# Kernel optimization log

Hardware: AMD Instinct MI355X
Metric: run time of the kernel (lower is better)

Reference implementation:

```python
import jax, jax.numpy as jnp
from jax import lax
import numpy as np

IMG_H, IMG_W = 800.0, 1344.0
NMS_PRE, NMS_POST, MAX_NUM = 2000, 1000, 1000
IOU_THR = 0.7
STRIDES = [4, 8, 16, 32, 64]
SIZES = [(200, 336), (100, 168), (50, 84), (25, 42), (13, 21)]
MAX_RATIO = float(abs(np.log(16.0 / 1000.0)))  # mmdet wh_ratio_clip


def _make_anchors(H, W, stride):
    # mmdet AnchorGenerator: scales=[8], ratios=[0.5,1,2], base_size=stride
    ratios = np.array([0.5, 1.0, 2.0])
    scale = 8.0
    hr = np.sqrt(ratios)
    wr = 1.0 / hr
    ws = stride * wr * scale
    hs = stride * hr * scale
    c = stride / 2.0
    base = np.stack([c - 0.5 * ws, c - 0.5 * hs, c + 0.5 * ws, c + 0.5 * hs], 1)  # [3,4]
    xx, yy = np.meshgrid(np.arange(W) * stride, np.arange(H) * stride)
    shifts = np.stack([xx, yy, xx, yy], -1).reshape(-1, 1, 4)  # [H*W,1,4]
    return (shifts + base[None]).reshape(-1, 4).astype(np.float32)  # order (H,W,A)


def setup_inputs() -> dict:
    key = jax.random.key(0)
    inp = {}
    for i, (H, W) in enumerate(SIZES):
        k1, k2, key = jax.random.split(key, 3)
        inp[f"cls{i}"] = jax.random.normal(k1, (2, 3, H, W), jnp.float32)
        inp[f"bbox{i}"] = jax.random.normal(k2, (2, 12, H, W), jnp.float32) * 0.5
        inp[f"anc{i}"] = jnp.asarray(_make_anchors(H, W, STRIDES[i]))
    return inp


def _delta2bbox(deltas, anchors):
    # deltas, anchors: [..., 4]; means=0, stds=1
    dx, dy = deltas[..., 0], deltas[..., 1]
    dw = jnp.clip(deltas[..., 2], -MAX_RATIO, MAX_RATIO)
    dh = jnp.clip(deltas[..., 3], -MAX_RATIO, MAX_RATIO)
    pw = anchors[..., 2] - anchors[..., 0]
    ph = anchors[..., 3] - anchors[..., 1]
    px = (anchors[..., 0] + anchors[..., 2]) * 0.5
    py = (anchors[..., 1] + anchors[..., 3]) * 0.5
    gw = pw * jnp.exp(dw)
    gh = ph * jnp.exp(dh)
    gx = px + pw * dx
    gy = py + ph * dy
    x1 = jnp.clip(gx - 0.5 * gw, 0.0, IMG_W)
    y1 = jnp.clip(gy - 0.5 * gh, 0.0, IMG_H)
    x2 = jnp.clip(gx + 0.5 * gw, 0.0, IMG_W)
    y2 = jnp.clip(gy + 0.5 * gh, 0.0, IMG_H)
    return jnp.stack([x1, y1, x2, y2], axis=-1)


def _pairwise_iou(b):
    # b: [N,4]
    area = (b[:, 2] - b[:, 0]) * (b[:, 3] - b[:, 1])
    lt = jnp.maximum(b[:, None, :2], b[None, :, :2])
    rb = jnp.minimum(b[:, None, 2:], b[None, :, 2:])
    wh = jnp.clip(rb - lt, 0.0, None)
    inter = wh[..., 0] * wh[..., 1]
    union = area[:, None] + area[None, :] - inter
    return inter / jnp.maximum(union, 1e-6)


def _nms_single(boxes, scores):
    # boxes [NMS_PRE,4], scores [NMS_PRE] (one image). Greedy NMS, keep NMS_POST.
    N = scores.shape[0]
    order = jnp.argsort(-scores)
    b = boxes[order]
    s = scores[order]
    iou = _pairwise_iou(lax.stop_gradient(b))
    idx = jnp.arange(N)

    def step(supp, i):
        keep_i = jnp.logical_not(supp[i])
        supp = supp | (keep_i & (iou[i] > IOU_THR) & (idx > i))
        return supp, keep_i

    _, keeps = lax.scan(step, jnp.zeros((N,), bool), idx)
    s_kept = jnp.where(keeps, s, -1.0)
    top_s, top_i = lax.top_k(s_kept, NMS_POST)
    return b[top_i], top_s


def _process_level(cls, bbox, anchors):
    B = cls.shape[0]
    # [B,A,H,W] -> [B,H,W,A] -> [B,N]; [B,A*4,H,W] -> [B,H,W,A*4] -> [B,N,4]
    scores = jax.nn.sigmoid(cls.transpose(0, 2, 3, 1).reshape(B, -1))
    deltas = bbox.transpose(0, 2, 3, 1).reshape(B, -1, 4)
    N = scores.shape[1]
    if N < NMS_PRE:  # pad small levels to min_num_bboxes (nms_pre)
        pad = NMS_PRE - N
        scores = jnp.pad(scores, ((0, 0), (0, pad)), constant_values=-1.0)
        deltas = jnp.pad(deltas, ((0, 0), (0, pad), (0, 0)))
        anchors = jnp.pad(anchors, ((0, pad), (0, 0)))
        top_s = scores
        top_i = jnp.broadcast_to(jnp.arange(NMS_PRE), (B, NMS_PRE))
    else:
        top_s, top_i = lax.top_k(scores, NMS_PRE)
    deltas_g = jnp.take_along_axis(deltas, top_i[..., None], axis=1)  # [B,NMS_PRE,4]
    anc_g = anchors[top_i]  # [B,NMS_PRE,4]
    props = _delta2bbox(deltas_g, anc_g)
    boxes, sc = jax.vmap(_nms_single)(props, top_s)
    return sc, boxes


def _forward(cls_list, bbox_list, anc_list):
    mlvl_scores, mlvl_props = [], []
    for cls, bbox, anc in zip(cls_list, bbox_list, anc_list):
        s, p = _process_level(cls, bbox, anc)
        mlvl_scores.append(s)
        mlvl_props.append(p)
    scores = jnp.concatenate(mlvl_scores, axis=1)      # [B, 5*NMS_POST]
    proposals = jnp.concatenate(mlvl_props, axis=1)    # [B, 5*NMS_POST, 4]
    _, topk_inds = lax.top_k(scores, MAX_NUM)
    return jnp.take_along_axis(proposals, topk_inds[..., None], axis=1)  # [B, MAX_NUM, 4]


def reference(cls0, cls1, cls2, cls3, cls4,
              bbox0, bbox1, bbox2, bbox3, bbox4,
              anc0, anc1, anc2, anc3, anc4):
    return _forward([cls0, cls1, cls2, cls3, cls4],
                    [bbox0, bbox1, bbox2, bbox3, bbox4],
                    [anc0, anc1, anc2, anc3, anc4])
```

## Files before the change

kernel.cpp:

```cpp
#include <hip/hip_runtime.h>
#include <cmath>


#define NPRE 2000
#define NPOST 1000

static __device__ __forceinline__ unsigned int flipf_dev(float f) {
  unsigned int u = __float_as_uint(f);
  return (u & 0x80000000u) ? ~u : (u | 0x80000000u);
}
static __device__ __forceinline__ float unflipf_dev(unsigned int k) {
  unsigned int u = (k & 0x80000000u) ? (k ^ 0x80000000u) : ~k;
  return __uint_as_float(u);
}
static __device__ __forceinline__ unsigned long long flip64_dev(double d) {
  unsigned long long u = (unsigned long long)__double_as_longlong(d);
  return (u & 0x8000000000000000ull) ? ~u : (u | 0x8000000000000000ull);
}

struct RPNParams {
  const float* cls[5];
  const float* bbox[5];
  const float* anc[5];
  unsigned int* hist;
  unsigned int* mainCount;
  unsigned int* candCount;
  unsigned int* Bstar;
  unsigned long long* mainEK;
  unsigned long long* candEK;
  unsigned long long* ekG;
  unsigned int* partialR;
  double* selBoxes;
  double* selScores;
  unsigned long long* mask;
  double* postScores;
  float* postBoxes;
  unsigned int* partial;
  float* out;
};

__device__ __constant__ int c_NL[5]  = {201600, 50400, 12600, 3150, 819};
__device__ __constant__ int c_HW[5]  = {67200, 16800, 4200, 1050, 273};
__device__ __constant__ int c_BPT[8] = {99, 99, 25, 25, 7, 7, 2, 2};

static __device__ __forceinline__ void map_block(int bx, int& t, int& chunk) {
  int start = 0;
  t = 0;
  for (int k = 0; k < 8; k++) {
    if (bx < start + c_BPT[k]) { t = k; break; }
    start += c_BPT[k];
  }
  chunk = bx - start;
}

__global__ void k_hist(RPNParams p) {
  int t, chunk;
  map_block(blockIdx.x, t, chunk);
  int l = t >> 1, b = t & 1;
  int N = c_NL[l], HW = c_HW[l];
  const float* cls = p.cls[l] + (size_t)b * 3 * HW;
  unsigned int* hist = p.hist + (size_t)t * 65536;
  int base = chunk * 2048 + threadIdx.x;
  for (int k = 0; k < 2; k++) {
    int n = base + k * 1024;
    if (n < N) {
      int a = n % 3, hw = n / 3;
      unsigned int key = flipf_dev(cls[a * HW + hw]);
      atomicAdd(&hist[key >> 16], 1u);
    }
  }
}

__global__ void k_find(RPNParams p) {
  int t = blockIdx.x;
  unsigned int* hist = p.hist + (size_t)t * 65536;
  __shared__ unsigned int S[1024];
  __shared__ unsigned int tail[64];
  __shared__ int gsel;
  __shared__ unsigned int baseAbove;
  int g = threadIdx.x;
  unsigned int s = 0;
  for (int j = 0; j < 64; j++) s += hist[g * 64 + j];
  S[g] = s;
  __syncthreads();
  for (int off = 1; off < 1024; off <<= 1) {
    unsigned int add = (g + off < 1024) ? S[g + off] : 0u;
    __syncthreads();
    S[g] += add;
    __syncthreads();
  }
  const unsigned int need = NPRE;
  if (S[g] >= need && (g == 1023 || S[g + 1] < need)) {
    gsel = g;
    baseAbove = (g == 1023) ? 0u : S[g + 1];
  }
  __syncthreads();
  if (threadIdx.x < 64) tail[threadIdx.x] = hist[gsel * 64 + threadIdx.x];
  __syncthreads();
  if (threadIdx.x == 0) {
    int gg = gsel;
    unsigned int c = baseAbove;
    int bstar = gg * 64;
    for (int bb = 63; bb >= 0; bb--) {
      c += tail[bb];
      if (c >= need) { bstar = gg * 64 + bb; break; }
    }
    p.Bstar[t] = (unsigned int)bstar;
  }
}

__global__ void k_compact(RPNParams p) {
  int t, chunk;
  map_block(blockIdx.x, t, chunk);
  int l = t >> 1, b = t & 1;
  int N = c_NL[l], HW = c_HW[l];
  const float* cls = p.cls[l] + (size_t)b * 3 * HW;
  unsigned int Bs = p.Bstar[t];
  int base = chunk * 2048 + threadIdx.x;
  for (int k = 0; k < 2; k++) {
    int n = base + k * 1024;
    if (n < N) {
      int a = n % 3, hw = n / 3;
      unsigned int key = flipf_dev(cls[a * HW + hw]);
      unsigned int hi = key >> 16;
      unsigned long long ek =
          ((unsigned long long)key << 32) | (unsigned int)(~(unsigned int)n);
      if (hi > Bs) {
        unsigned int pos = atomicAdd(&p.mainCount[t], 1u);
        if (pos < 2048u) p.mainEK[(size_t)t * 2048 + pos] = ek;
      } else if (hi == Bs) {
        unsigned int pos = atomicAdd(&p.candCount[t], 1u);
        if (pos < 8192u) p.candEK[(size_t)t * 8192 + pos] = ek;
      }
    }
  }
}

__global__ void k_fill(RPNParams p) {
  int t = blockIdx.x;
  int l = t >> 1, b = t & 1;
  int N = c_NL[l], HW = c_HW[l];
  int tid = threadIdx.x;
  unsigned long long* ekG = p.ekG + (size_t)t * 2048;
  if (N >= NPRE) {
    unsigned int cGT = min(p.mainCount[t], 2000u);
    unsigned int nC = min(p.candCount[t], 8192u);
    unsigned int needIn = 2000u - cGT;
    for (unsigned int m = tid; m < cGT; m += 256)
      ekG[m] = p.mainEK[(size_t)t * 2048 + m];
    const unsigned long long* cek = p.candEK + (size_t)t * 8192;
    for (unsigned int e = tid; e < nC; e += 256) {
      unsigned long long ve = cek[e];
      unsigned int r = 0;
      for (unsigned int j = 0; j < nC; j++) r += (cek[j] > ve) ? 1u : 0u;
      if (r < needIn) ekG[cGT + r] = ve;
    }
    for (unsigned int r = 2000u + tid; r < 2048u; r += 256)
      ekG[r] = (unsigned long long)(unsigned int)(~r);
  } else {
    const float* cls = p.cls[l] + (size_t)b * 3 * HW;
    for (int r = tid; r < 2048; r += 256) {
      if (r < N) {
        int a = r % 3, hw = r / 3;
        unsigned int key = flipf_dev(cls[a * HW + hw]);
        ekG[r] = ((unsigned long long)key << 32) |
                 (unsigned int)(~(unsigned int)r);
      } else {
        ekG[r] = (unsigned long long)(unsigned int)(~(unsigned int)r);
      }
    }
  }
}

__global__ void k_rank(RPNParams p) {
  int t = blockIdx.x >> 3;
  int s = blockIdx.x & 7;
  int tid = threadIdx.x;
  __shared__ unsigned long long sl[256];
  const unsigned long long* ekG = p.ekG + (size_t)t * 2048;
  sl[tid] = ekG[s * 256 + tid];
  __syncthreads();
  unsigned long long ve[8];
  unsigned int r[8];
#pragma unroll
  for (int k = 0; k < 8; k++) {
    ve[k] = ekG[k * 256 + tid];
    r[k] = 0;
  }
  for (int j = 0; j < 256; j++) {
    unsigned long long vj = sl[j];
#pragma unroll
    for (int k = 0; k < 8; k++) r[k] += (vj > ve[k]) ? 1u : 0u;
  }
  unsigned int* out = p.partialR + ((size_t)t * 8 + s) * 2048;
#pragma unroll
  for (int k = 0; k < 8; k++) out[k * 256 + tid] = r[k];
}

__global__ void k_scatter(RPNParams p) {
  int t = blockIdx.x;
  int l = t >> 1, b = t & 1;
  int HW = c_HW[l];
  int tid = threadIdx.x;
  __shared__ unsigned long long srt[2048];
  const unsigned long long* ekG = p.ekG + (size_t)t * 2048;
  for (int e = tid; e < 2048; e += 1024) {
    unsigned int rk = 0;
#pragma unroll
    for (int s = 0; s < 8; s++)
      rk += p.partialR[((size_t)t * 8 + s) * 2048 + e];
    srt[rk] = ekG[e];
  }
  __syncthreads();

  const double RCLIP = fabs(log(16.0 / 1000.0));
  const float* bbx = p.bbox[l] + (size_t)b * 12 * HW;
  const float* anc = p.anc[l];
  for (int r = tid; r < NPRE; r += 1024) {
    unsigned long long v = srt[r];
    unsigned int key = (unsigned int)(v >> 32);
    double* SB = p.selBoxes + ((size_t)t * NPRE + r) * 4;
    if (key == 0u) {
      SB[0] = 0.0; SB[1] = 0.0; SB[2] = 0.0; SB[3] = 0.0;
      p.selScores[(size_t)t * NPRE + r] = -1.0;
    } else {
      unsigned int idx = ~(unsigned int)(v & 0xFFFFFFFFull);
      int a = (int)(idx % 3u);
      int hw = (int)(idx / 3u);
      double d0 = (double)bbx[(a * 4 + 0) * HW + hw];
      double d1 = (double)bbx[(a * 4 + 1) * HW + hw];
      double d2 = (double)bbx[(a * 4 + 2) * HW + hw];
      double d3 = (double)bbx[(a * 4 + 3) * HW + hw];
      double a0 = (double)anc[(size_t)idx * 4 + 0];
      double a1 = (double)anc[(size_t)idx * 4 + 1];
      double a2 = (double)anc[(size_t)idx * 4 + 2];
      double a3 = (double)anc[(size_t)idx * 4 + 3];
      double dw = fmin(fmax(d2, -RCLIP), RCLIP);
      double dh = fmin(fmax(d3, -RCLIP), RCLIP);
      double pw = a2 - a0, ph = a3 - a1;
      double px = (a0 + a2) * 0.5, py = (a1 + a3) * 0.5;
      double gw = pw * exp(dw), gh = ph * exp(dh);
      double gx = px + pw * d0, gy = py + ph * d1;
      double x1 = fmin(fmax(gx - 0.5 * gw, 0.0), 1344.0);
      double y1 = fmin(fmax(gy - 0.5 * gh, 0.0), 800.0);
      double x2 = fmin(fmax(gx + 0.5 * gw, 0.0), 1344.0);
      double y2 = fmin(fmax(gy + 0.5 * gh, 0.0), 800.0);
      SB[0] = x1; SB[1] = y1; SB[2] = x2; SB[3] = y2;
      float f = unflipf_dev(key);
      p.selScores[(size_t)t * NPRE + r] = 1.0 / (1.0 + exp(-(double)f));
    }
  }
}

__global__ __launch_bounds__(640) void k_iou(RPNParams p) {
  int bx = blockIdx.x;
  int t = bx / 25;
  int q = bx % 25;
  __shared__ float X1[2048], Y1[2048], X2[2048], Y2[2048], AR[2048];
  const double* SB = p.selBoxes + (size_t)t * NPRE * 4;
  for (int i = threadIdx.x; i < 2048; i += 640) {
    float x1 = 0.f, y1 = 0.f, x2 = 0.f, y2 = 0.f;
    if (i < NPRE) {
      x1 = (float)SB[i * 4 + 0]; y1 = (float)SB[i * 4 + 1];
      x2 = (float)SB[i * 4 + 2]; y2 = (float)SB[i * 4 + 3];
    }
    X1[i] = x1; Y1[i] = y1; X2[i] = x2; Y2[i] = y2;
    AR[i] = (x2 - x1) * (y2 - y1);
  }
  __syncthreads();
  int wave = threadIdx.x >> 6, lane = threadIdx.x & 63;
  int g = q + 25 * wave;
  int i0 = g * 8;
  float x1i[8], y1i[8], x2i[8], y2i[8], ai[8];
#pragma unroll
  for (int r = 0; r < 8; r++) {
    int i = i0 + r;
    x1i[r] = X1[i]; y1i[r] = Y1[i]; x2i[r] = X2[i]; y2i[r] = Y2[i];
    ai[r] = AR[i];
  }
  int c0 = i0 >> 6;
  int j0 = c0 * 64 + lane;
  float cx1 = X1[j0], cy1 = Y1[j0], cx2 = X2[j0], cy2 = Y2[j0], car = AR[j0];
  for (int k = c0; k < 32; k++) {
    float nx1 = 0.f, ny1 = 0.f, nx2 = 0.f, ny2 = 0.f, nar = 0.f;
    if (k + 1 < 32) {
      int jn = (k + 1) * 64 + lane;
      nx1 = X1[jn]; ny1 = Y1[jn]; nx2 = X2[jn]; ny2 = Y2[jn];
      nar = AR[jn];
    }
    int j = k * 64 + lane;
    bool jin = j < NPRE;
    bool pred[8], need[8];
    bool needAny = false;
#pragma unroll
    for (int r = 0; r < 8; r++) {
      int i = i0 + r;
      bool valid = jin && (j > i);
      float lx = fmaxf(x1i[r], cx1), ly = fmaxf(y1i[r], cy1);
      float rx = fminf(x2i[r], cx2), ry = fminf(y2i[r], cy2);
      float w = fmaxf(rx - lx, 0.0f), h = fmaxf(ry - ly, 0.0f);
      float inter = w * h;
      float uni = fmaxf(ai[r] + car - inter, 1e-6f);
      float diff = inter - 0.7f * uni;
      pred[r] = valid && (diff > 0.0f);
      need[r] = valid && (fabsf(diff) <= 4.0f + 1e-5f * uni);
      needAny |= need[r];
    }
    if (__any(needAny)) {
#pragma unroll
      for (int r = 0; r < 8; r++) {
        if (need[r]) {
          int i = i0 + r;
          double a0 = SB[i * 4 + 0], b0 = SB[i * 4 + 1];
          double a2 = SB[i * 4 + 2], b2 = SB[i * 4 + 3];
          double c0d = SB[j * 4 + 0], d0 = SB[j * 4 + 1];
          double c2 = SB[j * 4 + 2], d2 = SB[j * 4 + 3];
          double dai = (a2 - a0) * (b2 - b0);
          double daj = (c2 - c0d) * (d2 - d0);
          double lxd = fmax(a0, c0d), lyd = fmax(b0, d0);
          double rxd = fmin(a2, c2), ryd = fmin(b2, d2);
          double wd = fmax(rxd - lxd, 0.0), hd = fmax(ryd - lyd, 0.0);
          double interd = wd * hd;
          double unid = fmax(dai + daj - interd, 1e-6);
          pred[r] = (interd / unid) > 0.7;
        }
      }
    }
#pragma unroll
    for (int r = 0; r < 8; r++) {
      unsigned long long word = __ballot(pred[r]);
      if (lane == 0) p.mask[((size_t)t * NPRE + i0 + r) * 32 + k] = word;
    }
    cx1 = nx1; cy1 = ny1; cx2 = nx2; cy2 = ny2; car = nar;
  }
}

#define GRP_N 63
#define RING 6
__global__ __launch_bounds__(512) void k_greedy(RPNParams p) {
  int t = blockIdx.x;
  int tid = threadIdx.x;
  __shared__ unsigned long long ring[RING * 1024];
  __shared__ int ready[GRP_N];
  __shared__ int cons_s;
  __shared__ unsigned long long kw[32], aw[32], bw[32];
  __shared__ unsigned int prefA[33], prefB[33];
  volatile int* rdy = ready;
  volatile int* cons = &cons_s;
  const unsigned long long* MK = p.mask + (size_t)t * NPRE * 32;
  for (int i = tid; i < GRP_N; i += 512) ready[i] = 0;
  if (tid == 0) cons_s = 0;
  __syncthreads();

  int wave = tid >> 6, lane = tid & 63;
  if (wave >= 1) {
    for (int g = wave - 1; g < GRP_N; g += 7) {
      while (g - *cons >= RING) __builtin_amdgcn_s_sleep(1);
      unsigned long long v[16];
#pragma unroll
      for (int k = 0; k < 16; k++) {
        int idx = k * 64 + lane;
        int row = g * 32 + (idx >> 5);
        v[k] = (row < NPRE) ? MK[(size_t)row * 32 + (idx & 31)] : 0ull;
      }
      int slot = g % RING;
#pragma unroll
      for (int k = 0; k < 16; k++)
        ring[slot * 1024 + k * 64 + lane] = v[k];
      __threadfence_block();
      if (lane == 0) rdy[g] = 1;
    }
  } else {
    unsigned long long supp = 0ull, keep = 0ull;
    for (int g = 0; g < GRP_N; g++) {
      while (rdy[g] == 0) { }
      __threadfence_block();
      int slot = g % RING;
      int c = g >> 1;
      int base = (g & 1) * 32;
      unsigned long long rv[32];
#pragma unroll
      for (int r = 0; r < 32; r++)
        rv[r] = ring[slot * 1024 + r * 32 + (lane & 31)];
      unsigned int sh = (unsigned int)(supp >> base);
      unsigned int s32 = (unsigned int)__builtin_amdgcn_readlane((int)sh, c);
      unsigned int kg = 0;
#pragma unroll
      for (int r = 0; r < 32; r++) {
        unsigned int rvh = (unsigned int)(rv[r] >> base);
        bool kp = (s32 & (1u << r)) == 0u;
        kg |= kp ? (1u << r) : 0u;
        s32 |= kp ? rvh : 0u;
      }
      kg = (unsigned int)__builtin_amdgcn_readlane((int)kg, c);
      unsigned long long acc0 = 0ull, acc1 = 0ull;
#pragma unroll
      for (int r = 0; r < 32; r += 2) {
        acc0 |= ((kg >> r) & 1u) ? rv[r] : 0ull;
        acc1 |= ((kg >> (r + 1)) & 1u) ? rv[r + 1] : 0ull;
      }
      supp |= acc0 | acc1;
      keep |= (lane == c) ? ((unsigned long long)kg << base) : 0ull;
      __threadfence_block();
      if (lane == 63) *cons = g + 1;
    }
    if (lane < 32) kw[lane] = keep;
  }
  __syncthreads();

  for (int ch = wave; ch < 32; ch += 8) {
    int i = ch * 64 + lane;
    bool inr = i < NPRE;
    bool kb = inr && ((kw[ch] >> lane) & 1ull);
    bool A = kb && (inr ? (p.selScores[(size_t)t * NPRE + i] > -0.5) : false);
    bool B = inr && !A;
    unsigned long long wa = __ballot(A);
    unsigned long long wb = __ballot(B);
    if (lane == 0) { aw[ch] = wa; bw[ch] = wb; }
  }
  __syncthreads();
  if (tid == 0) {
    unsigned int ca = 0, cb = 0;
    for (int w = 0; w < 32; w++) {
      prefA[w] = ca; ca += __popcll(aw[w]);
      prefB[w] = cb; cb += __popcll(bw[w]);
    }
    prefA[32] = ca; prefB[32] = cb;
  }
  __syncthreads();
  unsigned int KA = prefA[32];
  for (int i = tid; i < NPRE; i += 512) {
    int w = i >> 6, bpos = i & 63;
    unsigned long long below = (bpos == 0) ? 0ull : (~0ull >> (64 - bpos));
    bool kb = (kw[w] >> bpos) & 1ull;
    double s = p.selScores[(size_t)t * NPRE + i];
    bool A = kb && (s > -0.5);
    unsigned int slot;
    double outs;
    if (A) {
      slot = prefA[w] + (unsigned int)__popcll(aw[w] & below);
      outs = s;
    } else {
      slot = KA + prefB[w] + (unsigned int)__popcll(bw[w] & below);
      outs = -1.0;
    }
    if (slot < NPOST) {
      p.postScores[(size_t)t * NPOST + slot] = outs;
      const double* SB = p.selBoxes + ((size_t)t * NPRE + i) * 4;
      float* PB = p.postBoxes + ((size_t)t * NPOST + slot) * 4;
      PB[0] = (float)SB[0]; PB[1] = (float)SB[1];
      PB[2] = (float)SB[2]; PB[3] = (float)SB[3];
    }
  }
}

__global__ void k_finalA(RPNParams p) {
  int bx = blockIdx.x;
  int b = bx / 80;
  int rem = bx % 80;
  int s = rem >> 2;
  int ec = rem & 3;
  int j0 = s * 256;
  __shared__ unsigned long long kj[256];
  int tid = threadIdx.x;
  {
    int e = j0 + tid;
    unsigned long long v = 0ull;
    if (e < 5000) {
      int l = e / 1000, slot = e - l * 1000;
      int t = l * 2 + b;
      v = flip64_dev(p.postScores[(size_t)t * NPOST + slot]);
    }
    kj[tid] = v;
  }
  __syncthreads();
  int eidx[5];
  unsigned long long ke[5];
  unsigned int r[5];
#pragma unroll
  for (int k = 0; k < 5; k++) {
    int e = ec * 1280 + k * 256 + tid;
    eidx[k] = (e < 5000) ? e : -1;
    if (eidx[k] >= 0) {
      int l = e / 1000, slot = e - l * 1000;
      int t = l * 2 + b;
      ke[k] = flip64_dev(p.postScores[(size_t)t * NPOST + slot]);
    } else {
      ke[k] = 0ull;
    }
    r[k] = 0;
  }
  for (int j = 0; j < 256; j++) {
    unsigned long long vj = kj[j];
    int jg = j0 + j;
#pragma unroll
    for (int k = 0; k < 5; k++)
      r[k] += (vj > ke[k] || (vj == ke[k] && jg < eidx[k])) ? 1u : 0u;
  }
#pragma unroll
  for (int k = 0; k < 5; k++)
    if (eidx[k] >= 0)
      p.partial[((size_t)b * 20 + s) * 5000 + eidx[k]] = r[k];
}

__global__ void k_finalB(RPNParams p) {
  int b = blockIdx.x / 5;
  int ch = blockIdx.x % 5;
  int tid = threadIdx.x;
  if (tid < 1000) {
    int e = ch * 1000 + tid;
    unsigned int r = 0;
#pragma unroll
    for (int s = 0; s < 20; s++)
      r += p.partial[((size_t)b * 20 + s) * 5000 + e];
    if (r < NPOST) {
      int l = e / 1000, slot = e - l * 1000;
      int t = l * 2 + b;
      const float* PB = p.postBoxes + ((size_t)t * NPOST + slot) * 4;
      float* O = p.out + ((size_t)b * NPOST + r) * 4;
      O[0] = PB[0]; O[1] = PB[1]; O[2] = PB[2]; O[3] = PB[3];
    }
  }
}

extern "C" void kernel_launch(void* const* d_in, const int* in_sizes, int n_in,
                              void* d_out, int out_size, void* d_ws,
                              size_t ws_size, hipStream_t stream) {
  RPNParams p;
  bool interleaved = (n_in >= 2) && (in_sizes[1] == 4 * in_sizes[0]);
  for (int l = 0; l < 5; l++) {
    if (interleaved) {
      p.cls[l]  = (const float*)d_in[3 * l + 0];
      p.bbox[l] = (const float*)d_in[3 * l + 1];
      p.anc[l]  = (const float*)d_in[3 * l + 2];
    } else {
      p.cls[l]  = (const float*)d_in[l];
      p.bbox[l] = (const float*)d_in[5 + l];
      p.anc[l]  = (const float*)d_in[10 + l];
    }
  }
  char* w = (char*)d_ws;
  size_t off = 0;
  auto alloc = [&](size_t bytes) {
    off = (off + 255) & ~(size_t)255;
    void* r = w + off;
    off += bytes;
    return r;
  };
  p.hist      = (unsigned int*)alloc((size_t)10 * 65536 * 4);
  p.mainCount = (unsigned int*)alloc(10 * 4);
  p.candCount = (unsigned int*)alloc(10 * 4);
  size_t zbytes = off;
  p.Bstar      = (unsigned int*)alloc(10 * 4);
  p.mainEK     = (unsigned long long*)alloc((size_t)10 * 2048 * 8);
  p.candEK     = (unsigned long long*)alloc((size_t)10 * 8192 * 8);
  p.ekG        = (unsigned long long*)alloc((size_t)10 * 2048 * 8);
  p.partialR   = (unsigned int*)alloc((size_t)10 * 8 * 2048 * 4);
  p.selBoxes   = (double*)alloc((size_t)10 * NPRE * 4 * 8);
  p.selScores  = (double*)alloc((size_t)10 * NPRE * 8);
  p.mask       = (unsigned long long*)alloc((size_t)10 * NPRE * 32 * 8);
  p.postScores = (double*)alloc((size_t)10 * NPOST * 8);
  p.postBoxes  = (float*)alloc((size_t)10 * NPOST * 4 * 4);
  p.partial    = (unsigned int*)alloc((size_t)2 * 20 * 5000 * 4);
  p.out = (float*)d_out;
  (void)ws_size; (void)out_size;

  hipMemsetAsync(d_ws, 0, zbytes, stream);
  k_hist<<<dim3(266), dim3(1024), 0, stream>>>(p);
  k_find<<<dim3(8), dim3(1024), 0, stream>>>(p);
  k_compact<<<dim3(266), dim3(1024), 0, stream>>>(p);
  k_fill<<<dim3(10), dim3(256), 0, stream>>>(p);
  k_rank<<<dim3(80), dim3(256), 0, stream>>>(p);
  k_scatter<<<dim3(10), dim3(1024), 0, stream>>>(p);
  k_iou<<<dim3(250), dim3(640), 0, stream>>>(p);
  k_greedy<<<dim3(10), dim3(512), 0, stream>>>(p);
  k_finalA<<<dim3(160), dim3(256), 0, stream>>>(p);
  k_finalB<<<dim3(10), dim3(1024), 0, stream>>>(p);
}
```

Baseline: 419.6 us.

## Use per-block shared-memory 12-bit histograms and tile candidate ranking through LDS

```diff
diff --git a/kernel.cpp b/kernel.cpp
--- a/kernel.cpp
+++ b/kernel.cpp
@@ -42,6 +42,7 @@
 __device__ __constant__ int c_NL[5]  = {201600, 50400, 12600, 3150, 819};
 __device__ __constant__ int c_HW[5]  = {67200, 16800, 4200, 1050, 273};
 __device__ __constant__ int c_BPT[8] = {99, 99, 25, 25, 7, 7, 2, 2};
+__device__ __constant__ int c_BPT12[8] = {25, 25, 7, 7, 2, 2, 1, 1};
 
 static __device__ __forceinline__ void map_block(int bx, int& t, int& chunk) {
   int start = 0;
@@ -52,58 +53,79 @@
   }
   chunk = bx - start;
 }
-
-__global__ void k_hist(RPNParams p) {
+static __device__ __forceinline__ void map_block12(int bx, int& t, int& chunk) {
+  int start = 0;
+  t = 0;
+  for (int k = 0; k < 8; k++) {
+    if (bx < start + c_BPT12[k]) { t = k; break; }
+    start += c_BPT12[k];
+  }
+  chunk = bx - start;
+}
+
+__global__ __launch_bounds__(1024) void k_hist(RPNParams p) {
+  __shared__ unsigned int lh[4096];
   int t, chunk;
-  map_block(blockIdx.x, t, chunk);
+  map_block12(blockIdx.x, t, chunk);
   int l = t >> 1, b = t & 1;
   int N = c_NL[l], HW = c_HW[l];
   const float* cls = p.cls[l] + (size_t)b * 3 * HW;
-  unsigned int* hist = p.hist + (size_t)t * 65536;
-  int base = chunk * 2048 + threadIdx.x;
-  for (int k = 0; k < 2; k++) {
+  int tid = threadIdx.x;
+  for (int i = tid; i < 4096; i += 1024) lh[i] = 0;
+  __syncthreads();
+  int base = chunk * 8192 + tid;
+#pragma unroll
+  for (int k = 0; k < 8; k++) {
     int n = base + k * 1024;
     if (n < N) {
       int a = n % 3, hw = n / 3;
       unsigned int key = flipf_dev(cls[a * HW + hw]);
-      atomicAdd(&hist[key >> 16], 1u);
-    }
-  }
+      atomicAdd(&lh[key >> 20], 1u);
+    }
+  }
+  __syncthreads();
+  unsigned int* hout = p.hist + (size_t)blockIdx.x * 4096;
+  for (int i = tid; i < 4096; i += 1024) hout[i] = lh[i];
 }
 
 __global__ void k_find(RPNParams p) {
   int t = blockIdx.x;
-  unsigned int* hist = p.hist + (size_t)t * 65536;
+  __shared__ unsigned int H[4096];
   __shared__ unsigned int S[1024];
-  __shared__ unsigned int tail[64];
   __shared__ int gsel;
   __shared__ unsigned int baseAbove;
-  int g = threadIdx.x;
-  unsigned int s = 0;
-  for (int j = 0; j < 64; j++) s += hist[g * 64 + j];
-  S[g] = s;
+  int tid = threadIdx.x;
+  int start = 0;
+  for (int k = 0; k < t; k++) start += c_BPT12[k];
+  int bpt = c_BPT12[t];
+  for (int bin = tid; bin < 4096; bin += 1024) {
+    unsigned int s = 0;
+    for (int bb = 0; bb < bpt; bb++)
+      s += p.hist[(size_t)(start + bb) * 4096 + bin];
+    H[bin] = s;
+  }
+  __syncthreads();
+  S[tid] = H[tid * 4] + H[tid * 4 + 1] + H[tid * 4 + 2] + H[tid * 4 + 3];
   __syncthreads();
   for (int off = 1; off < 1024; off <<= 1) {
-    unsigned int add = (g + off < 1024) ? S[g + off] : 0u;
+    unsigned int add = (tid + off < 1024) ? S[tid + off] : 0u;
     __syncthreads();
-    S[g] += add;
+    S[tid] += add;
     __syncthreads();
   }
   const unsigned int need = NPRE;
-  if (S[g] >= need && (g == 1023 || S[g + 1] < need)) {
-    gsel = g;
-    baseAbove = (g == 1023) ? 0u : S[g + 1];
-  }
-  __syncthreads();
-  if (threadIdx.x < 64) tail[threadIdx.x] = hist[gsel * 64 + threadIdx.x];
-  __syncthreads();
-  if (threadIdx.x == 0) {
+  if (S[tid] >= need && (tid == 1023 || S[tid + 1] < need)) {
+    gsel = tid;
+    baseAbove = (tid == 1023) ? 0u : S[tid + 1];
+  }
+  __syncthreads();
+  if (tid == 0) {
     int gg = gsel;
     unsigned int c = baseAbove;
-    int bstar = gg * 64;
-    for (int bb = 63; bb >= 0; bb--) {
-      c += tail[bb];
-      if (c >= need) { bstar = gg * 64 + bb; break; }
+    int bstar = gg * 4;
+    for (int bb = 3; bb >= 0; bb--) {
+      c += H[gg * 4 + bb];
+      if (c >= need) { bstar = gg * 4 + bb; break; }
     }
     p.Bstar[t] = (unsigned int)bstar;
   }
@@ -122,7 +144,7 @@
     if (n < N) {
       int a = n % 3, hw = n / 3;
       unsigned int key = flipf_dev(cls[a * HW + hw]);
-      unsigned int hi = key >> 16;
+      unsigned int hi = key >> 20;
       unsigned long long ek =
           ((unsigned long long)key << 32) | (unsigned int)(~(unsigned int)n);
       if (hi > Bs) {
@@ -149,14 +171,35 @@
     for (unsigned int m = tid; m < cGT; m += 256)
       ekG[m] = p.mainEK[(size_t)t * 2048 + m];
     const unsigned long long* cek = p.candEK + (size_t)t * 8192;
-    for (unsigned int e = tid; e < nC; e += 256) {
-      unsigned long long ve = cek[e];
-      unsigned int r = 0;
-      for (unsigned int j = 0; j < nC; j++) r += (cek[j] > ve) ? 1u : 0u;
-      if (r < needIn) ekG[cGT + r] = ve;
-    }
-    for (unsigned int r = 2000u + tid; r < 2048u; r += 256)
-      ekG[r] = (unsigned long long)(unsigned int)(~r);
+    __shared__ unsigned long long sl[256];
+    for (unsigned int estrip = 0; estrip < nC; estrip += 2048) {
+      unsigned long long ve[8];
+      unsigned int r[8];
+      bool en[8];
+#pragma unroll
+      for (int k = 0; k < 8; k++) {
+        unsigned int e = estrip + k * 256 + tid;
+        en[k] = e < nC;
+        ve[k] = en[k] ? cek[e] : 0ull;
+        r[k] = 0;
+      }
+      for (unsigned int jb = 0; jb < nC; jb += 256) {
+        __syncthreads();
+        sl[tid] = (jb + tid < nC) ? cek[jb + tid] : 0ull;
+        __syncthreads();
+        int lim = (int)min(256u, nC - jb);
+        for (int j = 0; j < lim; j++) {
+          unsigned long long vj = sl[j];
+#pragma unroll
+          for (int k = 0; k < 8; k++) r[k] += (vj > ve[k]) ? 1u : 0u;
+        }
+      }
+#pragma unroll
+      for (int k = 0; k < 8; k++)
+        if (en[k] && r[k] < needIn) ekG[cGT + r[k]] = ve[k];
+    }
+    for (unsigned int r2 = 2000u + tid; r2 < 2048u; r2 += 256)
+      ekG[r2] = (unsigned long long)(unsigned int)(~r2);
   } else {
     const float* cls = p.cls[l] + (size_t)b * 3 * HW;
     for (int r = tid; r < 2048; r += 256) {
@@ -547,10 +590,10 @@
     off += bytes;
     return r;
   };
-  p.hist      = (unsigned int*)alloc((size_t)10 * 65536 * 4);
   p.mainCount = (unsigned int*)alloc(10 * 4);
   p.candCount = (unsigned int*)alloc(10 * 4);
   size_t zbytes = off;
+  p.hist       = (unsigned int*)alloc((size_t)70 * 4096 * 4);
   p.Bstar      = (unsigned int*)alloc(10 * 4);
   p.mainEK     = (unsigned long long*)alloc((size_t)10 * 2048 * 8);
   p.candEK     = (unsigned long long*)alloc((size_t)10 * 8192 * 8);
@@ -566,7 +609,7 @@
   (void)ws_size; (void)out_size;
 
   hipMemsetAsync(d_ws, 0, zbytes, stream);
-  k_hist<<<dim3(266), dim3(1024), 0, stream>>>(p);
+  k_hist<<<dim3(70), dim3(1024), 0, stream>>>(p);
   k_find<<<dim3(8), dim3(1024), 0, stream>>>(p);
   k_compact<<<dim3(266), dim3(1024), 0, stream>>>(p);
   k_fill<<<dim3(10), dim3(256), 0, stream>>>(p);
```

Result: slower. 467.3 us (+11.4%).
